# Kernel tuning notes

Measured on AMD Instinct MI355X. Metric: run time of the kernel, lower is better.

The kernel has to match this reference:

```python
import jax, jax.numpy as jnp
import numpy as np

N_NODES = 200000
N_EDGES = 800000
N_GRAPHS = 4096
IN_FEAT = 64
CONV_SIZES = [128, 128, 256, 256]
MAX_DEGREE = 5  # buckets 0..5 (degree clamped)
N_CLASSES = 2


def setup_inputs() -> dict:
    key = jax.random.key(0)
    ks = jax.random.split(key, 32)
    inp = {}
    inp["x"] = jax.random.normal(ks[0], (N_NODES, IN_FEAT), dtype=jnp.float32)
    inp["edge_index"] = jax.random.randint(ks[1], (2, N_EDGES), 0, N_NODES, dtype=jnp.int32)
    inp["batch"] = jnp.sort(jax.random.randint(ks[2], (N_NODES,), 0, N_GRAPHS, dtype=jnp.int32))
    # per-layer MFConv params: Wl (neighbor-sum branch, with bias), Wr (root branch, no bias),
    # one linear per degree bucket -> leading dim MAX_DEGREE+1
    c_in = IN_FEAT
    k = 3
    for li, c_out in enumerate(CONV_SIZES):
        s = 1.0 / np.sqrt(c_in)
        inp[f"Wl{li}"] = jax.random.normal(ks[k], (MAX_DEGREE + 1, c_in, c_out), dtype=jnp.float32) * s; k += 1
        inp[f"bl{li}"] = jax.random.normal(ks[k], (MAX_DEGREE + 1, c_out), dtype=jnp.float32) * 0.01; k += 1
        inp[f"Wr{li}"] = jax.random.normal(ks[k], (MAX_DEGREE + 1, c_in, c_out), dtype=jnp.float32) * s; k += 1
        c_in = c_out
    in_final = sum(CONV_SIZES) + CONV_SIZES[-1]  # concat of all layer outputs + pooled last layer
    inp["Wf"] = jax.random.normal(ks[k], (in_final, N_CLASSES), dtype=jnp.float32) * (1.0 / np.sqrt(in_final)); k += 1
    inp["bf"] = jax.random.normal(ks[k], (N_CLASSES,), dtype=jnp.float32) * 0.01
    return inp


def _mfconv(x, src, dst, deg, Wl, bl, Wr):
    # neighbor sum aggregation (source_to_target flow): msg_i = sum_{j->i} x_j
    msg = jax.ops.segment_sum(x[src], dst, num_segments=x.shape[0])  # [N, c_in]
    out = jnp.zeros((x.shape[0], Wl.shape[2]), dtype=x.dtype)
    for d in range(Wl.shape[0]):  # small fixed loop over degree buckets
        r = msg @ Wl[d] + bl[d] + x @ Wr[d]
        out = jnp.where((deg == d)[:, None], r, out)
    return out


def reference(x, edge_index, batch,
              Wl0, bl0, Wr0, Wl1, bl1, Wr1, Wl2, bl2, Wr2, Wl3, bl3, Wr3,
              Wf, bf):
    src, dst = edge_index[0], edge_index[1]
    n = x.shape[0]
    deg = jnp.clip(jnp.zeros((n,), jnp.int32).at[dst].add(1), 0, MAX_DEGREE)
    hs = []
    h = x
    for Wl, bl, Wr in ((Wl0, bl0, Wr0), (Wl1, bl1, Wr1), (Wl2, bl2, Wr2), (Wl3, bl3, Wr3)):
        h = _mfconv(h, src, dst, deg, Wl, bl, Wr)
        hs.append(h)
    # global_add_pool then repeat_interleave back to nodes == gather pooled by batch id
    h_pool = jax.ops.segment_sum(h, batch, num_segments=N_GRAPHS)  # [G, c_last]
    h_pool_ = h_pool[batch]  # [N, c_last]
    h_cat = jnp.concatenate(hs + [h_pool_], axis=1)  # [N, sum(sizes)+c_last]
    logits = h_cat @ Wf + bf
    return jax.nn.softmax(logits, axis=1)
```

## Files before the change

### kernel.cpp

```cpp
#include <hip/hip_runtime.h>
#include <cstdint>
#include <cstddef>

namespace {

constexpr int NN   = 200000;
constexpr int NE   = 800000;
constexpr int NG   = 4096;
constexpr int MAXD = 5;

constexpr int BM = 64;
constexpr int NBC = (NN + 255) / 256;
constexpr int NBLK  = (NN + BM - 1) / BM + 6;
constexpr int PERMN = NBLK * BM;

typedef _Float16 half8 __attribute__((ext_vector_type(8)));
typedef _Float16 half4 __attribute__((ext_vector_type(4)));
typedef _Float16 half2 __attribute__((ext_vector_type(2)));
typedef float    f32x4 __attribute__((ext_vector_type(4)));

constexpr size_t P_L0 = (size_t)6 * 128 * 128;
constexpr size_t P_L1 = (size_t)6 * 256 * 128;
constexpr size_t P_L2 = (size_t)6 * 256 * 256;
constexpr size_t P_L3 = (size_t)6 * 512 * 256;
constexpr size_t O_P0 = 0;
constexpr size_t O_P1 = O_P0 + P_L0;
constexpr size_t O_P2 = O_P1 + P_L1;
constexpr size_t O_P3 = O_P2 + P_L2;
constexpr size_t WTOT = O_P3 + P_L3;


__global__ void k_memset32(int* __restrict__ p, int v, int n) {
    int i = blockIdx.x * 256 + threadIdx.x;
    if (i < n) p[i] = v;
}

__global__ void k_report(float* __restrict__ outp, float v, int n) {
    int i = blockIdx.x * 256 + threadIdx.x;
    if (i < n) outp[i] = v;
}

template <int CIN, int COUT>
__global__ void k_wpack(const float* __restrict__ Wl, const float* __restrict__ Wr,
                        _Float16* __restrict__ hi, _Float16* __restrict__ lo) {
    constexpr int NT = CIN / 16;
    constexpr int NB = COUT / 16;
    const int total = 6 * NT * NB * 64;
    int idx = blockIdx.x * 256 + threadIdx.x;
    if (idx >= total) return;
    const int lane = idx & 63;
    int rest = idx >> 6;
    const int nb = rest % NB; rest /= NB;
    const int ti = rest % NT;
    const int d  = rest / NT;
    const int k0 = ti * 32 + ((lane >> 4) * 8);
    const int n  = nb * 16 + (lane & 15);
    half8 hv, lv;
#pragma unroll
    for (int j = 0; j < 8; j++) {
        const int kk = k0 + j;
        const float v = (kk < CIN)
                            ? Wl[((size_t)d * CIN + kk) * COUT + n]
                            : Wr[((size_t)d * CIN + (kk - CIN)) * COUT + n];
        const _Float16 h = (_Float16)v;
        hv[j] = h;
        lv[j] = (_Float16)(v - (float)h);
    }
    *(half8*)(hi + (size_t)idx * 8) = hv;
    *(half8*)(lo + (size_t)idx * 8) = lv;
}


__global__ void k_count_deg(const int* __restrict__ dst, int* __restrict__ deg) {
    int e = blockIdx.x * 256 + threadIdx.x;
    if (e < NE) atomicAdd(&deg[dst[e]], 1);
}

__global__ void k_scan_part(const int* __restrict__ deg, int* __restrict__ part) {
    __shared__ int s[256];
    int t = threadIdx.x, i = blockIdx.x * 256 + t;
    s[t] = (i < NN) ? deg[i] : 0;
    __syncthreads();
    for (int st = 128; st > 0; st >>= 1) {
        if (t < st) s[t] += s[t + st];
        __syncthreads();
    }
    if (t == 0) part[blockIdx.x] = s[0];
}

__global__ void k_scan_single(int* __restrict__ part, int nb) {
    __shared__ int s[1024];
    int t = threadIdx.x;
    int v0 = (t < nb) ? part[t] : 0;
    s[t] = v0;
    __syncthreads();
    for (int off = 1; off < 1024; off <<= 1) {
        int v = (t >= off) ? s[t - off] : 0;
        __syncthreads();
        s[t] += v;
        __syncthreads();
    }
    if (t < nb) part[t] = s[t] - v0;
}

__global__ void k_scan_final(const int* __restrict__ deg, const int* __restrict__ part,
                             int* __restrict__ row_ptr, int* __restrict__ cursor) {
    __shared__ int s[256];
    int t = threadIdx.x, i = blockIdx.x * 256 + t;
    int v0 = (i < NN) ? deg[i] : 0;
    s[t] = v0;
    __syncthreads();
    for (int off = 1; off < 256; off <<= 1) {
        int v = (t >= off) ? s[t - off] : 0;
        __syncthreads();
        s[t] += v;
        __syncthreads();
    }
    if (i < NN) {
        int excl = s[t] - v0 + part[blockIdx.x];
        row_ptr[i] = excl;
        cursor[i]  = excl;
        if (i == NN - 1) row_ptr[NN] = excl + v0;
    }
}

__global__ void k_fill_csr(const int* __restrict__ src, const int* __restrict__ dst,
                           int* __restrict__ cursor, int* __restrict__ col) {
    int e = blockIdx.x * 256 + threadIdx.x;
    if (e < NE) {
        int d = dst[e];
        int slot = atomicAdd(&cursor[d], 1);
        col[slot] = src[e];
    }
}


__global__ void k_bucket_blockcount(const int* __restrict__ deg, int* __restrict__ blkcnt) {
    __shared__ int h[6];
    int t = threadIdx.x;
    if (t < 6) h[t] = 0;
    __syncthreads();
    int i = blockIdx.x * 256 + t;
    if (i < NN) atomicAdd(&h[min(deg[i], MAXD)], 1);
    __syncthreads();
    if (t < 6) blkcnt[t * NBC + blockIdx.x] = h[t];
}

__global__ void k_bucket_scanall(int* __restrict__ blkcnt, int* __restrict__ bpad) {
    __shared__ int tot[6];
    int t = threadIdx.x;
    if (t < 6) {
        int run = 0;
        for (int j = 0; j < NBC; j++) {
            int v = blkcnt[t * NBC + j];
            blkcnt[t * NBC + j] = run;
            run += v;
        }
        tot[t] = run;
    }
    __syncthreads();
    if (t == 0) {
        int off = 0;
        for (int b = 0; b < 6; b++) {
            bpad[b] = off;
            off += ((tot[b] + BM - 1) / BM) * BM;
        }
        bpad[6] = off;
    }
}

__global__ void k_scatter2(const int* __restrict__ deg, const int* __restrict__ blkcnt,
                           const int* __restrict__ bpad, int* __restrict__ perm) {
    __shared__ int base[6];
    int t = threadIdx.x;
    if (t < 6) base[t] = bpad[t] + blkcnt[t * NBC + blockIdx.x];
    __syncthreads();
    int i = blockIdx.x * 256 + t;
    if (i < NN) {
        int b = min(deg[i], MAXD);
        int pos = atomicAdd(&base[b], 1);
        perm[pos] = i;
    }
}


__global__ void k_aggregate128(const float* __restrict__ hin, const int* __restrict__ row_ptr,
                               const int* __restrict__ col, float* __restrict__ msg) {
    int node = blockIdx.x * 4 + (threadIdx.x >> 6);
    int lane = threadIdx.x & 63;
    int s = row_ptr[node], e = row_ptr[node + 1];
    float2 acc = make_float2(0.f, 0.f);
    int p = s;
    for (; p + 4 <= e; p += 4) {
        const int c0 = col[p], c1 = col[p + 1], c2 = col[p + 2], c3 = col[p + 3];
        const float2 v0 = *(const float2*)(hin + (size_t)c0 * 128 + lane * 2);
        const float2 v1 = *(const float2*)(hin + (size_t)c1 * 128 + lane * 2);
        const float2 v2 = *(const float2*)(hin + (size_t)c2 * 128 + lane * 2);
        const float2 v3 = *(const float2*)(hin + (size_t)c3 * 128 + lane * 2);
        acc.x += (v0.x + v1.x) + (v2.x + v3.x);
        acc.y += (v0.y + v1.y) + (v2.y + v3.y);
    }
    for (; p < e; p++) {
        const float2 v = *(const float2*)(hin + (size_t)col[p] * 128 + lane * 2);
        acc.x += v.x; acc.y += v.y;
    }
    *(float2*)(msg + (size_t)node * 128 + lane * 2) = acc;
}

template <int C0, int C1, int COUT, int MINW, bool POOL_FUSE>
__launch_bounds__(512, MINW)
__global__ void k_transform(const float* __restrict__ hin0, const float* __restrict__ hin1,
                            const int* __restrict__ row_ptr, const int* __restrict__ col,
                            const _Float16* __restrict__ wph, const _Float16* __restrict__ wpl,
                            const float* __restrict__ bias, const float* __restrict__ Wf,
                            const int* __restrict__ perm, const int* __restrict__ deg,
                            const int* __restrict__ batch,
                            float* __restrict__ out0, float* __restrict__ pool,
                            float* __restrict__ logits, int wf_off) {
    constexpr int CIN = C0 + C1;
    constexpr int NW  = CIN / 32;
    constexpr int NT  = 2 * NW;
    constexpr int NB  = COUT / 16;
    constexpr int NTN = NB / 8;
    constexpr int CPL = CIN / 64;
    constexpr int PB_R = POOL_FUSE ? 64 : 1;
    constexpr int PB_C = 258;

    struct FragBuf {
        _Float16 Ah[NW][4][64][8];
        _Float16 Al[NW][4][64][8];
    };
    union SMemU {
        FragBuf f;
        float pbuf[PB_R][PB_C];
    };
    __shared__ SMemU sm;
    __shared__ int rowid[BM];
    __shared__ int gb[BM];
    __shared__ float lsx[8][BM], lsy[8][BM];

    const int t  = threadIdx.x;
    const int m0 = blockIdx.x * BM;

    if (t < BM) rowid[t] = perm[m0 + t];
    __syncthreads();
    if (rowid[0] < 0) return;

    const int d = min(deg[rowid[0]], MAXD);

    const int am = t & 63, wv = t >> 6;

    if constexpr (POOL_FUSE) {
        if (t < BM) gb[t] = (rowid[t] >= 0) ? batch[rowid[t]] : -1;
    }

    const int kk = CPL * am;
    const bool lo_half = (C1 == 0) || (kk < C0);
    const float* gsrc = lo_half ? hin0 : hin1;
    const int    gst  = lo_half ? C0 : C1;
    const int    goff = lo_half ? kk : (kk - C0);
    const int ti0 = kk >> 5;
    const int o0  = (kk >> 3) & 3;
    const int j00 = kk & 7;

    {
#pragma unroll
        for (int i = 0; i < 8; i++) {
            const int r = wv * 8 + i;
            const int node = rowid[r];
            float a0 = 0.f, a1 = 0.f, a2 = 0.f, a3 = 0.f;
            if (node >= 0) {
                const int es = row_ptr[node], ee = row_ptr[node + 1];
                int p = es;
                for (; p + 4 <= ee; p += 4) {
                    const int c0 = col[p], c1 = col[p + 1];
                    const int c2 = col[p + 2], c3 = col[p + 3];
                    const float* r0 = gsrc + (size_t)c0 * gst + goff;
                    const float* r1 = gsrc + (size_t)c1 * gst + goff;
                    const float* r2 = gsrc + (size_t)c2 * gst + goff;
                    const float* r3 = gsrc + (size_t)c3 * gst + goff;
                    if constexpr (CPL == 4) {
                        f32x4 v0 = *(const f32x4*)r0, v1 = *(const f32x4*)r1;
                        f32x4 v2 = *(const f32x4*)r2, v3 = *(const f32x4*)r3;
                        v0 += v1; v2 += v3; v0 += v2;
                        a0 += v0[0]; a1 += v0[1]; a2 += v0[2]; a3 += v0[3];
                    } else if constexpr (CPL == 2) {
                        float2 v0 = *(const float2*)r0, v1 = *(const float2*)r1;
                        float2 v2 = *(const float2*)r2, v3 = *(const float2*)r3;
                        a0 += (v0.x + v1.x) + (v2.x + v3.x);
                        a1 += (v0.y + v1.y) + (v2.y + v3.y);
                    } else {
                        a0 += (*r0 + *r1) + (*r2 + *r3);
                    }
                }
                for (; p < ee; p++) {
                    const float* rr = gsrc + (size_t)col[p] * gst + goff;
                    if constexpr (CPL == 4) {
                        f32x4 v = *(const f32x4*)rr;
                        a0 += v[0]; a1 += v[1]; a2 += v[2]; a3 += v[3];
                    } else if constexpr (CPL == 2) {
                        float2 v = *(const float2*)rr;
                        a0 += v.x; a1 += v.y;
                    } else {
                        a0 += *rr;
                    }
                }
            }
            const int mt = r >> 4, rl = r & 15;
            if constexpr (CPL == 4) {
                half4 hv, lv;
                hv[0] = (_Float16)a0; lv[0] = (_Float16)(a0 - (float)hv[0]);
                hv[1] = (_Float16)a1; lv[1] = (_Float16)(a1 - (float)hv[1]);
                hv[2] = (_Float16)a2; lv[2] = (_Float16)(a2 - (float)hv[2]);
                hv[3] = (_Float16)a3; lv[3] = (_Float16)(a3 - (float)hv[3]);
                *(half4*)&sm.f.Ah[ti0][mt][rl + 16 * o0][j00] = hv;
                *(half4*)&sm.f.Al[ti0][mt][rl + 16 * o0][j00] = lv;
            } else if constexpr (CPL == 2) {
                half2 hv, lv;
                hv[0] = (_Float16)a0; lv[0] = (_Float16)(a0 - (float)hv[0]);
                hv[1] = (_Float16)a1; lv[1] = (_Float16)(a1 - (float)hv[1]);
                *(half2*)&sm.f.Ah[ti0][mt][rl + 16 * o0][j00] = hv;
                *(half2*)&sm.f.Al[ti0][mt][rl + 16 * o0][j00] = lv;
            } else {
                const _Float16 h = (_Float16)a0;
                sm.f.Ah[ti0][mt][rl + 16 * o0][j00] = h;
                sm.f.Al[ti0][mt][rl + 16 * o0][j00] = (_Float16)(a0 - (float)h);
            }
        }
    }
    __syncthreads();

    const int lx = t & 15, qd = (t >> 4) & 3;
    const int nb0 = wv * NTN;

    f32x4 acc[4][NTN];
#pragma unroll
    for (int mt = 0; mt < 4; mt++)
#pragma unroll
        for (int nt = 0; nt < NTN; nt++) acc[mt][nt] = (f32x4)0.f;

    for (int ti = 0; ti < NW; ti++) {
        half8 bh[NTN], bl[NTN];
        const size_t tbase = (((size_t)d * NT + ti) * NB) * 512;
#pragma unroll
        for (int nt = 0; nt < NTN; nt++) {
            const size_t off = tbase + (size_t)(nb0 + nt) * 512 + (size_t)am * 8;
            bh[nt] = *(const half8*)(wph + off);
            bl[nt] = *(const half8*)(wpl + off);
        }
        half8 ah[4], alo[4];
#pragma unroll
        for (int mt = 0; mt < 4; mt++) {
            ah[mt]  = *(const half8*)&sm.f.Ah[ti][mt][am][0];
            alo[mt] = *(const half8*)&sm.f.Al[ti][mt][am][0];
        }
#pragma unroll
        for (int nt = 0; nt < NTN; nt++)
#pragma unroll
            for (int mt = 0; mt < 4; mt++) {
                acc[mt][nt] = __builtin_amdgcn_mfma_f32_16x16x32_f16(ah[mt],  bh[nt], acc[mt][nt], 0, 0, 0);
                acc[mt][nt] = __builtin_amdgcn_mfma_f32_16x16x32_f16(alo[mt], bh[nt], acc[mt][nt], 0, 0, 0);
                acc[mt][nt] = __builtin_amdgcn_mfma_f32_16x16x32_f16(ah[mt],  bl[nt], acc[mt][nt], 0, 0, 0);
            }
    }
    __syncthreads();

    {
#pragma unroll
        for (int i = 0; i < 8; i++) {
            const int r = wv * 8 + i;
            const int node = rowid[r];
            const int mt = r >> 4, rl = r & 15;
            if constexpr (CPL == 4) {
                f32x4 v = (f32x4)0.f;
                if (node >= 0) v = *(const f32x4*)(gsrc + (size_t)node * gst + goff);
                half4 hv, lv;
#pragma unroll
                for (int c = 0; c < 4; c++) {
                    const _Float16 h = (_Float16)v[c];
                    hv[c] = h; lv[c] = (_Float16)(v[c] - (float)h);
                }
                *(half4*)&sm.f.Ah[ti0][mt][rl + 16 * o0][j00] = hv;
                *(half4*)&sm.f.Al[ti0][mt][rl + 16 * o0][j00] = lv;
            } else if constexpr (CPL == 2) {
                float2 v = make_float2(0.f, 0.f);
                if (node >= 0) v = *(const float2*)(gsrc + (size_t)node * gst + goff);
                half2 hv, lv;
                hv[0] = (_Float16)v.x; lv[0] = (_Float16)(v.x - (float)hv[0]);
                hv[1] = (_Float16)v.y; lv[1] = (_Float16)(v.y - (float)hv[1]);
                *(half2*)&sm.f.Ah[ti0][mt][rl + 16 * o0][j00] = hv;
                *(half2*)&sm.f.Al[ti0][mt][rl + 16 * o0][j00] = lv;
            } else {
                float v = 0.f;
                if (node >= 0) v = gsrc[(size_t)node * gst + goff];
                const _Float16 h = (_Float16)v;
                sm.f.Ah[ti0][mt][rl + 16 * o0][j00] = h;
                sm.f.Al[ti0][mt][rl + 16 * o0][j00] = (_Float16)(v - (float)h);
            }
        }
    }
    __syncthreads();

    for (int ti = 0; ti < NW; ti++) {
        half8 bh[NTN], bl[NTN];
        const size_t tbase = (((size_t)d * NT + NW + ti) * NB) * 512;
#pragma unroll
        for (int nt = 0; nt < NTN; nt++) {
            const size_t off = tbase + (size_t)(nb0 + nt) * 512 + (size_t)am * 8;
            bh[nt] = *(const half8*)(wph + off);
            bl[nt] = *(const half8*)(wpl + off);
        }
        half8 ah[4], alo[4];
#pragma unroll
        for (int mt = 0; mt < 4; mt++) {
            ah[mt]  = *(const half8*)&sm.f.Ah[ti][mt][am][0];
            alo[mt] = *(const half8*)&sm.f.Al[ti][mt][am][0];
        }
#pragma unroll
        for (int nt = 0; nt < NTN; nt++)
#pragma unroll
            for (int mt = 0; mt < 4; mt++) {
                acc[mt][nt] = __builtin_amdgcn_mfma_f32_16x16x32_f16(ah[mt],  bh[nt], acc[mt][nt], 0, 0, 0);
                acc[mt][nt] = __builtin_amdgcn_mfma_f32_16x16x32_f16(alo[mt], bh[nt], acc[mt][nt], 0, 0, 0);
                acc[mt][nt] = __builtin_amdgcn_mfma_f32_16x16x32_f16(ah[mt],  bl[nt], acc[mt][nt], 0, 0, 0);
            }
    }

    float blv[NTN], w0[NTN], w1[NTN];
    int cols[NTN];
#pragma unroll
    for (int nt = 0; nt < NTN; nt++) {
        cols[nt] = wv * (16 * NTN) + nt * 16 + lx;
        blv[nt] = bias[d * COUT + cols[nt]];
        w0[nt]  = Wf[(size_t)(wf_off + cols[nt]) * 2 + 0];
        w1[nt]  = Wf[(size_t)(wf_off + cols[nt]) * 2 + 1];
    }

    __syncthreads();

#pragma unroll
    for (int mt = 0; mt < 4; mt++)
#pragma unroll
    for (int r = 0; r < 4; r++) {
        const int ri = mt * 16 + qd * 4 + r;
        const int node = rowid[ri];
        float p0 = 0.f, p1 = 0.f;
        float h[NTN];
#pragma unroll
        for (int nt = 0; nt < NTN; nt++) h[nt] = 0.f;
        if (node >= 0) {
#pragma unroll
            for (int nt = 0; nt < NTN; nt++) {
                h[nt] = acc[mt][nt][r] + blv[nt];
                p0 = fmaf(h[nt], w0[nt], p0);
                p1 = fmaf(h[nt], w1[nt], p1);
            }
            if constexpr (!POOL_FUSE) {
                float* orow = out0 + (size_t)node * COUT;
#pragma unroll
                for (int nt = 0; nt < NTN; nt++) orow[cols[nt]] = h[nt];
            }
        }
        if constexpr (POOL_FUSE) {
#pragma unroll
            for (int nt = 0; nt < NTN; nt++) sm.pbuf[ri][cols[nt]] = h[nt];
        }
#pragma unroll
        for (int s = 1; s < 16; s <<= 1) {
            p0 += __shfl_xor(p0, s, 64);
            p1 += __shfl_xor(p1, s, 64);
        }
        if (lx == 0) {
            lsx[wv][ri] = p0;
            lsy[wv][ri] = p1;
        }
    }
    __syncthreads();

    if (t < BM) {
        const int node = rowid[t];
        if (node >= 0) {
            float sx = 0.f, sy = 0.f;
#pragma unroll
            for (int w = 0; w < 8; w++) { sx += lsx[w][t]; sy += lsy[w][t]; }
            logits[(size_t)node * 2 + 0] += sx;
            logits[(size_t)node * 2 + 1] += sy;
        }
    }

    if constexpr (POOL_FUSE) {
        const int c  = t & 255;
        const int rh = t >> 8;
        float run = 0.f;
        int rg = -1;
        const int r0 = rh * 32, r1 = r0 + 32;
        for (int r = r0; r < r1; r++) {
            const int g = gb[r];
            if (g != rg) {
                if (rg >= 0) atomicAdd(&pool[(size_t)rg * 256 + c], run);
                run = 0.f; rg = g;
            }
            if (g >= 0) run += sm.pbuf[r][c];
        }
        if (rg >= 0) atomicAdd(&pool[(size_t)rg * 256 + c], run);
    }
}


__launch_bounds__(512, 4)
__global__ void k_gemm2b(float* __restrict__ buf0, float* __restrict__ buf1,
                         const _Float16* __restrict__ wph, const _Float16* __restrict__ wpl,
                         const float* __restrict__ bias, const float* __restrict__ Wf,
                         const int* __restrict__ perm, const int* __restrict__ deg,
                         float* __restrict__ logits) {
    constexpr int COUT = 256, NT = 8, NB = 16, NTN = 2;
    __shared__ _Float16 Ah[NT][4][64][8];
    __shared__ _Float16 Al[NT][4][64][8];
    __shared__ int rowid[BM];
    __shared__ float lsx[8][BM], lsy[8][BM];

    const int t  = threadIdx.x;
    const int m0 = blockIdx.x * BM;

    if (t < BM) rowid[t] = perm[m0 + t];
    __syncthreads();
    if (rowid[0] < 0) return;

    const int d = min(deg[rowid[0]], MAXD);

    const int am = t & 63, wv = t >> 6;

    {
        const int kk = 4 * am;
        const float* gsrc = (am < 32) ? buf0 : buf1;
        const int    goff = (am < 32) ? kk : (kk - 128);
        const int ti = am >> 3;
        const int o  = (am >> 1) & 3;
        const int j0 = 4 * (am & 1);
#pragma unroll
        for (int i = 0; i < 8; i++) {
            const int r = wv * 8 + i;
            const int node = rowid[r];
            f32x4 v = (f32x4)0.f;
            if (node >= 0) v = *(const f32x4*)(gsrc + (size_t)node * 128 + goff);
            const int mt = r >> 4, rl = r & 15;
            half4 hv, lv;
#pragma unroll
            for (int c = 0; c < 4; c++) {
                const _Float16 h = (_Float16)v[c];
                hv[c] = h; lv[c] = (_Float16)(v[c] - (float)h);
            }
            *(half4*)&Ah[ti][mt][rl + 16 * o][j0] = hv;
            *(half4*)&Al[ti][mt][rl + 16 * o][j0] = lv;
        }
    }
    __syncthreads();

    const int lx = t & 15, qd = (t >> 4) & 3;
    const int nb0 = wv * NTN;

    f32x4 acc[4][NTN];
#pragma unroll
    for (int mt = 0; mt < 4; mt++)
#pragma unroll
        for (int nt = 0; nt < NTN; nt++) acc[mt][nt] = (f32x4)0.f;

    for (int ti = 0; ti < NT; ti++) {
        half8 bh[NTN], bl[NTN];
        const size_t tbase = (((size_t)d * NT + ti) * NB) * 512;
#pragma unroll
        for (int nt = 0; nt < NTN; nt++) {
            const size_t off = tbase + (size_t)(nb0 + nt) * 512 + (size_t)am * 8;
            bh[nt] = *(const half8*)(wph + off);
            bl[nt] = *(const half8*)(wpl + off);
        }
        half8 ah[4], alo[4];
#pragma unroll
        for (int mt = 0; mt < 4; mt++) {
            ah[mt]  = *(const half8*)&Ah[ti][mt][am][0];
            alo[mt] = *(const half8*)&Al[ti][mt][am][0];
        }
#pragma unroll
        for (int nt = 0; nt < NTN; nt++)
#pragma unroll
            for (int mt = 0; mt < 4; mt++) {
                acc[mt][nt] = __builtin_amdgcn_mfma_f32_16x16x32_f16(ah[mt],  bh[nt], acc[mt][nt], 0, 0, 0);
                acc[mt][nt] = __builtin_amdgcn_mfma_f32_16x16x32_f16(alo[mt], bh[nt], acc[mt][nt], 0, 0, 0);
                acc[mt][nt] = __builtin_amdgcn_mfma_f32_16x16x32_f16(ah[mt],  bl[nt], acc[mt][nt], 0, 0, 0);
            }
    }

    float blv[NTN], w0[NTN], w1[NTN];
    int cols[NTN];
#pragma unroll
    for (int nt = 0; nt < NTN; nt++) {
        cols[nt] = wv * 32 + nt * 16 + lx;
        blv[nt] = bias[d * COUT + cols[nt]];
        w0[nt]  = Wf[(size_t)(256 + cols[nt]) * 2 + 0];
        w1[nt]  = Wf[(size_t)(256 + cols[nt]) * 2 + 1];
    }
#pragma unroll
    for (int mt = 0; mt < 4; mt++)
#pragma unroll
    for (int r = 0; r < 4; r++) {
        const int ri = mt * 16 + qd * 4 + r;
        const int node = rowid[ri];
        float p0 = 0.f, p1 = 0.f;
        if (node >= 0) {
#pragma unroll
            for (int nt = 0; nt < NTN; nt++) {
                const float h = acc[mt][nt][r] + blv[nt];
                p0 = fmaf(h, w0[nt], p0);
                p1 = fmaf(h, w1[nt], p1);
                if (cols[nt] < 128) buf0[(size_t)node * 128 + cols[nt]] = h;
                else                buf1[(size_t)node * 128 + cols[nt] - 128] = h;
            }
        }
#pragma unroll
        for (int s = 1; s < 16; s <<= 1) {
            p0 += __shfl_xor(p0, s, 64);
            p1 += __shfl_xor(p1, s, 64);
        }
        if (lx == 0) {
            lsx[wv][ri] = p0;
            lsy[wv][ri] = p1;
        }
    }
    __syncthreads();
    if (t < BM) {
        const int node = rowid[t];
        if (node >= 0) {
            float sx = 0.f, sy = 0.f;
#pragma unroll
            for (int w = 0; w < 8; w++) { sx += lsx[w][t]; sy += lsy[w][t]; }
            logits[(size_t)node * 2 + 0] += sx;
            logits[(size_t)node * 2 + 1] += sy;
        }
    }
}


__global__ void k_pool_logits(const float* __restrict__ pool, const float* __restrict__ Wf,
                              const float* __restrict__ bf, float* __restrict__ pl) {
    int g = blockIdx.x * 4 + (threadIdx.x >> 6);
    int lane = threadIdx.x & 63;
    const float* pr = pool + (size_t)g * 256;
    float p0 = 0.f, p1 = 0.f;
#pragma unroll
    for (int j = 0; j < 4; j++) {
        int k = lane + 64 * j;
        float v = pr[k];
        p0 = fmaf(v, Wf[(size_t)(768 + k) * 2 + 0], p0);
        p1 = fmaf(v, Wf[(size_t)(768 + k) * 2 + 1], p1);
    }
#pragma unroll
    for (int s = 1; s < 64; s <<= 1) {
        p0 += __shfl_xor(p0, s, 64);
        p1 += __shfl_xor(p1, s, 64);
    }
    if (lane == 0) {
        pl[(size_t)g * 2 + 0] = p0 + bf[0];
        pl[(size_t)g * 2 + 1] = p1 + bf[1];
    }
}

__global__ void k_final(const float* __restrict__ logits, const float* __restrict__ pl,
                        const int* __restrict__ batch, float* __restrict__ outp) {
    int i = blockIdx.x * 256 + threadIdx.x;
    if (i < NN) {
        int g = batch[i];
        float l0 = logits[(size_t)i * 2 + 0] + pl[(size_t)g * 2 + 0];
        float l1 = logits[(size_t)i * 2 + 1] + pl[(size_t)g * 2 + 1];
        float m = fmaxf(l0, l1);
        float e0 = expf(l0 - m), e1 = expf(l1 - m);
        float inv = 1.f / (e0 + e1);
        outp[(size_t)i * 2 + 0] = e0 * inv;
        outp[(size_t)i * 2 + 1] = e1 * inv;
    }
}

}

extern "C" void kernel_launch(void* const* d_in, const int* in_sizes, int n_in,
                              void* d_out, int out_size, void* d_ws, size_t ws_size,
                              hipStream_t stream) {
    const float* x     = (const float*)d_in[0];
    const int*   ei    = (const int*)d_in[1];
    const int*   batch = (const int*)d_in[2];
    const float* Wl0 = (const float*)d_in[3];  const float* bl0 = (const float*)d_in[4];
    const float* Wr0 = (const float*)d_in[5];
    const float* Wl1 = (const float*)d_in[6];  const float* bl1 = (const float*)d_in[7];
    const float* Wr1 = (const float*)d_in[8];
    const float* Wl2 = (const float*)d_in[9];  const float* bl2 = (const float*)d_in[10];
    const float* Wr2 = (const float*)d_in[11];
    const float* Wl3 = (const float*)d_in[12]; const float* bl3 = (const float*)d_in[13];
    const float* Wr3 = (const float*)d_in[14];
    const float* Wf  = (const float*)d_in[15]; const float* bf  = (const float*)d_in[16];
    const int* src = ei;
    const int* dst = ei + NE;
    float* outp = (float*)d_out;
    (void)in_sizes; (void)n_in;

    char* w = (char*)d_ws;
    auto alloc = [&](size_t bytes) -> void* {
        void* p = (void*)w;
        w += (bytes + 255) & ~(size_t)255;
        return p;
    };
    int*   deg    = (int*)alloc((size_t)NN * 4);
    float* logits = (float*)alloc((size_t)NN * 2 * 4);
    float* pool   = (float*)alloc((size_t)NG * 256 * 4);
    size_t zero_words = (size_t)(w - (char*)deg) / 4;
    int*   bpad    = (int*)alloc(32);
    int*   blkcnt  = (int*)alloc((size_t)6 * NBC * 4);
    int*   perm    = (int*)alloc((size_t)PERMN * 4);
    int*   row_ptr = (int*)alloc((size_t)(NN + 1) * 4);
    int*   cursor  = (int*)alloc((size_t)NN * 4);
    int*   col     = (int*)alloc((size_t)NE * 4);
    int*   part    = (int*)alloc(1024 * 4);
    float* pl      = (float*)alloc((size_t)NG * 2 * 4);
    _Float16* whi  = (_Float16*)alloc(WTOT * 2);
    _Float16* wlo  = (_Float16*)alloc(WTOT * 2);
    float* bufA    = (float*)alloc((size_t)NN * 128 * 4);
    float* bufB    = (float*)alloc((size_t)NN * 128 * 4);

    size_t required = (size_t)(w - (char*)d_ws);
    if (required > ws_size) {
        k_report<<<(out_size + 255) / 256, 256, 0, stream>>>(
            outp, (float)(double)(ws_size >> 20), out_size);
        return;
    }

    dim3 b256(256);
    dim3 b512(512);
    k_memset32<<<(int)((zero_words + 255) / 256), b256, 0, stream>>>((int*)deg, 0, (int)zero_words);
    k_memset32<<<(PERMN + 255) / 256, b256, 0, stream>>>(perm, -1, PERMN);

    k_wpack<64, 128><<<(int)(P_L0 / 8 + 255) / 256, b256, 0, stream>>>(Wl0, Wr0, whi + O_P0, wlo + O_P0);
    k_wpack<128, 128><<<(int)(P_L1 / 8 + 255) / 256, b256, 0, stream>>>(Wl1, Wr1, whi + O_P1, wlo + O_P1);
    k_wpack<128, 256><<<(int)(P_L2 / 8 + 255) / 256, b256, 0, stream>>>(Wl2, Wr2, whi + O_P2, wlo + O_P2);
    k_wpack<256, 256><<<(int)(P_L3 / 8 + 255) / 256, b256, 0, stream>>>(Wl3, Wr3, whi + O_P3, wlo + O_P3);

    k_count_deg<<<NE / 256, b256, 0, stream>>>(dst, deg);
    k_scan_part<<<NBC, b256, 0, stream>>>(deg, part);
    k_scan_single<<<1, 1024, 0, stream>>>(part, NBC);
    k_scan_final<<<NBC, b256, 0, stream>>>(deg, part, row_ptr, cursor);
    k_fill_csr<<<NE / 256, b256, 0, stream>>>(src, dst, cursor, col);
    k_bucket_blockcount<<<NBC, b256, 0, stream>>>(deg, blkcnt);
    k_bucket_scanall<<<1, 64, 0, stream>>>(blkcnt, bpad);
    k_scatter2<<<NBC, b256, 0, stream>>>(deg, blkcnt, bpad, perm);

    k_transform<64, 0, 128, 4, false><<<dim3(NBLK), b512, 0, stream>>>(
        x, nullptr, row_ptr, col, whi + O_P0, wlo + O_P0,
        bl0, Wf, perm, deg, nullptr, bufA, nullptr, logits, 0);
    k_transform<128, 0, 128, 4, false><<<dim3(NBLK), b512, 0, stream>>>(
        bufA, nullptr, row_ptr, col, whi + O_P1, wlo + O_P1,
        bl1, Wf, perm, deg, nullptr, bufB, nullptr, logits, 128);
    k_aggregate128<<<NN / 4, b256, 0, stream>>>(bufB, row_ptr, col, bufA);
    k_gemm2b<<<dim3(NBLK), b512, 0, stream>>>(
        bufA, bufB, whi + O_P2, wlo + O_P2, bl2, Wf, perm, deg, logits);
    k_transform<128, 128, 256, 4, true><<<dim3(NBLK), b512, 0, stream>>>(
        bufA, bufB, row_ptr, col, whi + O_P3, wlo + O_P3,
        bl3, Wf, perm, deg, batch, nullptr, pool, logits, 512);

    k_pool_logits<<<NG / 4, b256, 0, stream>>>(pool, Wf, bf, pl);
    k_final<<<NBC, b256, 0, stream>>>(logits, pl, batch, outp);
}
```

Before: 1.209 ms.

## Split K-dimension staging into 128-wide phases to shrink LDS and raise occupancy

The transform and gemm2b kernels now stage the A operand through shared memory in 128-column phases instead of the full input width. This cuts the LDS footprint, and the pooling buffer is halved to 32 rows processed in two passes. Launch bounds rise from 4 to 8 waves per SIMD, aiming for more resident blocks to hide gather latency. In exchange there are extra barriers per phase, the neighbor gathers are repeated once per phase, and fewer registers are available per thread, which could cause spills.

```diff
diff --git a/kernel.cpp b/kernel.cpp
--- a/kernel.cpp
+++ b/kernel.cpp
@@ -222,13 +222,16 @@
     constexpr int NT  = 2 * NW;
     constexpr int NB  = COUT / 16;
     constexpr int NTN = NB / 8;
-    constexpr int CPL = CIN / 64;
-    constexpr int PB_R = POOL_FUSE ? 64 : 1;
+    constexpr int PHW = (CIN >= 128) ? (CIN / 128) : 1;
+    constexpr int KW  = CIN / PHW;
+    constexpr int CPLp = KW / 64;
+    constexpr int NWP = KW / 32;
+    constexpr int PB_R = POOL_FUSE ? 32 : 1;
     constexpr int PB_C = 258;
 
     struct FragBuf {
-        _Float16 Ah[NW][4][64][8];
-        _Float16 Al[NW][4][64][8];
+        _Float16 Ah[NWP][4][64][8];
+        _Float16 Al[NWP][4][64][8];
     };
     union SMemU {
         FragBuf f;
@@ -254,37 +257,40 @@
         if (t < BM) gb[t] = (rowid[t] >= 0) ? batch[rowid[t]] : -1;
     }
 
-    const int kk = CPL * am;
-    const bool lo_half = (C1 == 0) || (kk < C0);
-    const float* gsrc = lo_half ? hin0 : hin1;
-    const int    gst  = lo_half ? C0 : C1;
-    const int    goff = lo_half ? kk : (kk - C0);
-    const int ti0 = kk >> 5;
-    const int o0  = (kk >> 3) & 3;
-    const int j00 = kk & 7;
-
-    {
+    const int kk  = CPLp * am;
+    const int tiL = kk >> 5;
+    const int oL  = (kk >> 3) & 3;
+    const int jL  = kk & 7;
+
+    const int lx = t & 15, qd = (t >> 4) & 3;
+    const int nb0 = wv * NTN;
+
+    f32x4 acc[4][NTN];
+#pragma unroll
+    for (int mt = 0; mt < 4; mt++)
+#pragma unroll
+        for (int nt = 0; nt < NTN; nt++) acc[mt][nt] = (f32x4)0.f;
+
+#pragma unroll
+    for (int p = 0; p < PHW; p++) {
+        const float* src = (C1 != 0 && p == 1) ? hin1 : hin0;
+        const int    str = (C1 != 0 && p == 1) ? C1 : C0;
 #pragma unroll
         for (int i = 0; i < 8; i++) {
             const int r = wv * 8 + i;
             const int node = rowid[r];
-            float a0 = 0.f, a1 = 0.f, a2 = 0.f, a3 = 0.f;
+            float a0 = 0.f, a1 = 0.f;
             if (node >= 0) {
                 const int es = row_ptr[node], ee = row_ptr[node + 1];
-                int p = es;
-                for (; p + 4 <= ee; p += 4) {
-                    const int c0 = col[p], c1 = col[p + 1];
-                    const int c2 = col[p + 2], c3 = col[p + 3];
-                    const float* r0 = gsrc + (size_t)c0 * gst + goff;
-                    const float* r1 = gsrc + (size_t)c1 * gst + goff;
-                    const float* r2 = gsrc + (size_t)c2 * gst + goff;
-                    const float* r3 = gsrc + (size_t)c3 * gst + goff;
-                    if constexpr (CPL == 4) {
-                        f32x4 v0 = *(const f32x4*)r0, v1 = *(const f32x4*)r1;
-                        f32x4 v2 = *(const f32x4*)r2, v3 = *(const f32x4*)r3;
-                        v0 += v1; v2 += v3; v0 += v2;
-                        a0 += v0[0]; a1 += v0[1]; a2 += v0[2]; a3 += v0[3];
-                    } else if constexpr (CPL == 2) {
+                int pp = es;
+                for (; pp + 4 <= ee; pp += 4) {
+                    const int c0 = col[pp], c1 = col[pp + 1];
+                    const int c2 = col[pp + 2], c3 = col[pp + 3];
+                    const float* r0 = src + (size_t)c0 * str + kk;
+                    const float* r1 = src + (size_t)c1 * str + kk;
+                    const float* r2 = src + (size_t)c2 * str + kk;
+                    const float* r3 = src + (size_t)c3 * str + kk;
+                    if constexpr (CPLp == 2) {
                         float2 v0 = *(const float2*)r0, v1 = *(const float2*)r1;
                         float2 v2 = *(const float2*)r2, v3 = *(const float2*)r3;
                         a0 += (v0.x + v1.x) + (v2.x + v3.x);
@@ -293,12 +299,9 @@
                         a0 += (*r0 + *r1) + (*r2 + *r3);
                     }
                 }
-                for (; p < ee; p++) {
-                    const float* rr = gsrc + (size_t)col[p] * gst + goff;
-                    if constexpr (CPL == 4) {
-                        f32x4 v = *(const f32x4*)rr;
-                        a0 += v[0]; a1 += v[1]; a2 += v[2]; a3 += v[3];
-                    } else if constexpr (CPL == 2) {
+                for (; pp < ee; pp++) {
+                    const float* rr = src + (size_t)col[pp] * str + kk;
+                    if constexpr (CPLp == 2) {
                         float2 v = *(const float2*)rr;
                         a0 += v.x; a1 += v.y;
                     } else {
@@ -307,123 +310,97 @@
                 }
             }
             const int mt = r >> 4, rl = r & 15;
-            if constexpr (CPL == 4) {
-                half4 hv, lv;
-                hv[0] = (_Float16)a0; lv[0] = (_Float16)(a0 - (float)hv[0]);
-                hv[1] = (_Float16)a1; lv[1] = (_Float16)(a1 - (float)hv[1]);
-                hv[2] = (_Float16)a2; lv[2] = (_Float16)(a2 - (float)hv[2]);
-                hv[3] = (_Float16)a3; lv[3] = (_Float16)(a3 - (float)hv[3]);
-                *(half4*)&sm.f.Ah[ti0][mt][rl + 16 * o0][j00] = hv;
-                *(half4*)&sm.f.Al[ti0][mt][rl + 16 * o0][j00] = lv;
-            } else if constexpr (CPL == 2) {
+            if constexpr (CPLp == 2) {
                 half2 hv, lv;
                 hv[0] = (_Float16)a0; lv[0] = (_Float16)(a0 - (float)hv[0]);
                 hv[1] = (_Float16)a1; lv[1] = (_Float16)(a1 - (float)hv[1]);
-                *(half2*)&sm.f.Ah[ti0][mt][rl + 16 * o0][j00] = hv;
-                *(half2*)&sm.f.Al[ti0][mt][rl + 16 * o0][j00] = lv;
+                *(half2*)&sm.f.Ah[tiL][mt][rl + 16 * oL][jL] = hv;
+                *(half2*)&sm.f.Al[tiL][mt][rl + 16 * oL][jL] = lv;
             } else {
                 const _Float16 h = (_Float16)a0;
-                sm.f.Ah[ti0][mt][rl + 16 * o0][j00] = h;
-                sm.f.Al[ti0][mt][rl + 16 * o0][j00] = (_Float16)(a0 - (float)h);
-            }
-        }
-    }
-    __syncthreads();
-
-    const int lx = t & 15, qd = (t >> 4) & 3;
-    const int nb0 = wv * NTN;
-
-    f32x4 acc[4][NTN];
-#pragma unroll
-    for (int mt = 0; mt < 4; mt++)
-#pragma unroll
-        for (int nt = 0; nt < NTN; nt++) acc[mt][nt] = (f32x4)0.f;
-
-    for (int ti = 0; ti < NW; ti++) {
-        half8 bh[NTN], bl[NTN];
-        const size_t tbase = (((size_t)d * NT + ti) * NB) * 512;
-#pragma unroll
-        for (int nt = 0; nt < NTN; nt++) {
-            const size_t off = tbase + (size_t)(nb0 + nt) * 512 + (size_t)am * 8;
-            bh[nt] = *(const half8*)(wph + off);
-            bl[nt] = *(const half8*)(wpl + off);
-        }
-        half8 ah[4], alo[4];
-#pragma unroll
-        for (int mt = 0; mt < 4; mt++) {
-            ah[mt]  = *(const half8*)&sm.f.Ah[ti][mt][am][0];
-            alo[mt] = *(const half8*)&sm.f.Al[ti][mt][am][0];
-        }
-#pragma unroll
-        for (int nt = 0; nt < NTN; nt++)
+                sm.f.Ah[tiL][mt][rl + 16 * oL][jL] = h;
+                sm.f.Al[tiL][mt][rl + 16 * oL][jL] = (_Float16)(a0 - (float)h);
+            }
+        }
+        __syncthreads();
+        for (int ti = 0; ti < NWP; ti++) {
+            half8 bh[NTN], bl[NTN];
+            const size_t tbase = (((size_t)d * NT + (p * NWP + ti)) * NB) * 512;
+#pragma unroll
+            for (int nt = 0; nt < NTN; nt++) {
+                const size_t off = tbase + (size_t)(nb0 + nt) * 512 + (size_t)am * 8;
+                bh[nt] = *(const half8*)(wph + off);
+                bl[nt] = *(const half8*)(wpl + off);
+            }
+            half8 ah[4], alo[4];
 #pragma unroll
             for (int mt = 0; mt < 4; mt++) {
-                acc[mt][nt] = __builtin_amdgcn_mfma_f32_16x16x32_f16(ah[mt],  bh[nt], acc[mt][nt], 0, 0, 0);
-                acc[mt][nt] = __builtin_amdgcn_mfma_f32_16x16x32_f16(alo[mt], bh[nt], acc[mt][nt], 0, 0, 0);
-                acc[mt][nt] = __builtin_amdgcn_mfma_f32_16x16x32_f16(ah[mt],  bl[nt], acc[mt][nt], 0, 0, 0);
-            }
-    }
-    __syncthreads();
-
-    {
+                ah[mt]  = *(const half8*)&sm.f.Ah[ti][mt][am][0];
+                alo[mt] = *(const half8*)&sm.f.Al[ti][mt][am][0];
+            }
+#pragma unroll
+            for (int nt = 0; nt < NTN; nt++)
+#pragma unroll
+                for (int mt = 0; mt < 4; mt++) {
+                    acc[mt][nt] = __builtin_amdgcn_mfma_f32_16x16x32_f16(ah[mt],  bh[nt], acc[mt][nt], 0, 0, 0);
+                    acc[mt][nt] = __builtin_amdgcn_mfma_f32_16x16x32_f16(alo[mt], bh[nt], acc[mt][nt], 0, 0, 0);
+                    acc[mt][nt] = __builtin_amdgcn_mfma_f32_16x16x32_f16(ah[mt],  bl[nt], acc[mt][nt], 0, 0, 0);
+                }
+        }
+        __syncthreads();
+    }
+
+#pragma unroll
+    for (int p = 0; p < PHW; p++) {
+        const float* src = (C1 != 0 && p == 1) ? hin1 : hin0;
+        const int    str = (C1 != 0 && p == 1) ? C1 : C0;
 #pragma unroll
         for (int i = 0; i < 8; i++) {
             const int r = wv * 8 + i;
             const int node = rowid[r];
             const int mt = r >> 4, rl = r & 15;
-            if constexpr (CPL == 4) {
-                f32x4 v = (f32x4)0.f;
-                if (node >= 0) v = *(const f32x4*)(gsrc + (size_t)node * gst + goff);
-                half4 hv, lv;
-#pragma unroll
-                for (int c = 0; c < 4; c++) {
-                    const _Float16 h = (_Float16)v[c];
-                    hv[c] = h; lv[c] = (_Float16)(v[c] - (float)h);
-                }
-                *(half4*)&sm.f.Ah[ti0][mt][rl + 16 * o0][j00] = hv;
-                *(half4*)&sm.f.Al[ti0][mt][rl + 16 * o0][j00] = lv;
-            } else if constexpr (CPL == 2) {
+            if constexpr (CPLp == 2) {
                 float2 v = make_float2(0.f, 0.f);
-                if (node >= 0) v = *(const float2*)(gsrc + (size_t)node * gst + goff);
+                if (node >= 0) v = *(const float2*)(src + (size_t)node * str + kk);
                 half2 hv, lv;
                 hv[0] = (_Float16)v.x; lv[0] = (_Float16)(v.x - (float)hv[0]);
                 hv[1] = (_Float16)v.y; lv[1] = (_Float16)(v.y - (float)hv[1]);
-                *(half2*)&sm.f.Ah[ti0][mt][rl + 16 * o0][j00] = hv;
-                *(half2*)&sm.f.Al[ti0][mt][rl + 16 * o0][j00] = lv;
+                *(half2*)&sm.f.Ah[tiL][mt][rl + 16 * oL][jL] = hv;
+                *(half2*)&sm.f.Al[tiL][mt][rl + 16 * oL][jL] = lv;
             } else {
                 float v = 0.f;
-                if (node >= 0) v = gsrc[(size_t)node * gst + goff];
+                if (node >= 0) v = src[(size_t)node * str + kk];
                 const _Float16 h = (_Float16)v;
-                sm.f.Ah[ti0][mt][rl + 16 * o0][j00] = h;
-                sm.f.Al[ti0][mt][rl + 16 * o0][j00] = (_Float16)(v - (float)h);
-            }
-        }
-    }
-    __syncthreads();
-
-    for (int ti = 0; ti < NW; ti++) {
-        half8 bh[NTN], bl[NTN];
-        const size_t tbase = (((size_t)d * NT + NW + ti) * NB) * 512;
-#pragma unroll
-        for (int nt = 0; nt < NTN; nt++) {
-            const size_t off = tbase + (size_t)(nb0 + nt) * 512 + (size_t)am * 8;
-            bh[nt] = *(const half8*)(wph + off);
-            bl[nt] = *(const half8*)(wpl + off);
-        }
-        half8 ah[4], alo[4];
-#pragma unroll
-        for (int mt = 0; mt < 4; mt++) {
-            ah[mt]  = *(const half8*)&sm.f.Ah[ti][mt][am][0];
-            alo[mt] = *(const half8*)&sm.f.Al[ti][mt][am][0];
-        }
-#pragma unroll
-        for (int nt = 0; nt < NTN; nt++)
+                sm.f.Ah[tiL][mt][rl + 16 * oL][jL] = h;
+                sm.f.Al[tiL][mt][rl + 16 * oL][jL] = (_Float16)(v - (float)h);
+            }
+        }
+        __syncthreads();
+        for (int ti = 0; ti < NWP; ti++) {
+            half8 bh[NTN], bl[NTN];
+            const size_t tbase = (((size_t)d * NT + (NW + p * NWP + ti)) * NB) * 512;
+#pragma unroll
+            for (int nt = 0; nt < NTN; nt++) {
+                const size_t off = tbase + (size_t)(nb0 + nt) * 512 + (size_t)am * 8;
+                bh[nt] = *(const half8*)(wph + off);
+                bl[nt] = *(const half8*)(wpl + off);
+            }
+            half8 ah[4], alo[4];
 #pragma unroll
             for (int mt = 0; mt < 4; mt++) {
-                acc[mt][nt] = __builtin_amdgcn_mfma_f32_16x16x32_f16(ah[mt],  bh[nt], acc[mt][nt], 0, 0, 0);
-                acc[mt][nt] = __builtin_amdgcn_mfma_f32_16x16x32_f16(alo[mt], bh[nt], acc[mt][nt], 0, 0, 0);
-                acc[mt][nt] = __builtin_amdgcn_mfma_f32_16x16x32_f16(ah[mt],  bl[nt], acc[mt][nt], 0, 0, 0);
-            }
+                ah[mt]  = *(const half8*)&sm.f.Ah[ti][mt][am][0];
+                alo[mt] = *(const half8*)&sm.f.Al[ti][mt][am][0];
+            }
+#pragma unroll
+            for (int nt = 0; nt < NTN; nt++)
+#pragma unroll
+                for (int mt = 0; mt < 4; mt++) {
+                    acc[mt][nt] = __builtin_amdgcn_mfma_f32_16x16x32_f16(ah[mt],  bh[nt], acc[mt][nt], 0, 0, 0);
+                    acc[mt][nt] = __builtin_amdgcn_mfma_f32_16x16x32_f16(alo[mt], bh[nt], acc[mt][nt], 0, 0, 0);
+                    acc[mt][nt] = __builtin_amdgcn_mfma_f32_16x16x32_f16(ah[mt],  bl[nt], acc[mt][nt], 0, 0, 0);
+                }
+        }
+        __syncthreads();
     }
 
     float blv[NTN], w0[NTN], w1[NTN];
@@ -436,8 +413,6 @@
         w1[nt]  = Wf[(size_t)(wf_off + cols[nt]) * 2 + 1];
     }
 
-    __syncthreads();
-
 #pragma unroll
     for (int mt = 0; mt < 4; mt++)
 #pragma unroll
@@ -445,25 +420,19 @@
         const int ri = mt * 16 + qd * 4 + r;
         const int node = rowid[ri];
         float p0 = 0.f, p1 = 0.f;
-        float h[NTN];
-#pragma unroll
-        for (int nt = 0; nt < NTN; nt++) h[nt] = 0.f;
         if (node >= 0) {
 #pragma unroll
             for (int nt = 0; nt < NTN; nt++) {
-                h[nt] = acc[mt][nt][r] + blv[nt];
-                p0 = fmaf(h[nt], w0[nt], p0);
-                p1 = fmaf(h[nt], w1[nt], p1);
+                const float h = acc[mt][nt][r] + blv[nt];
+                p0 = fmaf(h, w0[nt], p0);
+                p1 = fmaf(h, w1[nt], p1);
             }
             if constexpr (!POOL_FUSE) {
                 float* orow = out0 + (size_t)node * COUT;
 #pragma unroll
-                for (int nt = 0; nt < NTN; nt++) orow[cols[nt]] = h[nt];
-            }
-        }
-        if constexpr (POOL_FUSE) {
-#pragma unroll
-            for (int nt = 0; nt < NTN; nt++) sm.pbuf[ri][cols[nt]] = h[nt];
+                for (int nt = 0; nt < NTN; nt++)
+                    orow[cols[nt]] = acc[mt][nt][r] + blv[nt];
+            }
         }
 #pragma unroll
         for (int s = 1; s < 16; s <<= 1) {
@@ -489,33 +458,51 @@
     }
 
     if constexpr (POOL_FUSE) {
-        const int c  = t & 255;
-        const int rh = t >> 8;
-        float run = 0.f;
-        int rg = -1;
-        const int r0 = rh * 32, r1 = r0 + 32;
-        for (int r = r0; r < r1; r++) {
-            const int g = gb[r];
-            if (g != rg) {
+#pragma unroll
+        for (int half = 0; half < 2; half++) {
+#pragma unroll
+            for (int mt = 2 * half; mt < 2 * half + 2; mt++)
+#pragma unroll
+            for (int r = 0; r < 4; r++) {
+                const int ri = mt * 16 + qd * 4 + r;
+                const int node = rowid[ri];
+#pragma unroll
+                for (int nt = 0; nt < NTN; nt++)
+                    sm.pbuf[ri - 32 * half][cols[nt]] =
+                        (node >= 0) ? (acc[mt][nt][r] + blv[nt]) : 0.f;
+            }
+            __syncthreads();
+            {
+                const int c  = t & 255;
+                const int rh = t >> 8;
+                float run = 0.f;
+                int rg = -1;
+                const int r0 = rh * 16, r1 = r0 + 16;
+                for (int rr = r0; rr < r1; rr++) {
+                    const int g = gb[32 * half + rr];
+                    if (g != rg) {
+                        if (rg >= 0) atomicAdd(&pool[(size_t)rg * 256 + c], run);
+                        run = 0.f; rg = g;
+                    }
+                    if (g >= 0) run += sm.pbuf[rr][c];
+                }
                 if (rg >= 0) atomicAdd(&pool[(size_t)rg * 256 + c], run);
-                run = 0.f; rg = g;
-            }
-            if (g >= 0) run += sm.pbuf[r][c];
-        }
-        if (rg >= 0) atomicAdd(&pool[(size_t)rg * 256 + c], run);
-    }
-}
-
-
-__launch_bounds__(512, 4)
+            }
+            __syncthreads();
+        }
+    }
+}
+
+
+__launch_bounds__(512, 8)
 __global__ void k_gemm2b(float* __restrict__ buf0, float* __restrict__ buf1,
                          const _Float16* __restrict__ wph, const _Float16* __restrict__ wpl,
                          const float* __restrict__ bias, const float* __restrict__ Wf,
                          const int* __restrict__ perm, const int* __restrict__ deg,
                          float* __restrict__ logits) {
-    constexpr int COUT = 256, NT = 8, NB = 16, NTN = 2;
-    __shared__ _Float16 Ah[NT][4][64][8];
-    __shared__ _Float16 Al[NT][4][64][8];
+    constexpr int COUT = 256, NT = 8, NB = 16, NTN = 2, NWP = 4;
+    __shared__ _Float16 Ah[NWP][4][64][8];
+    __shared__ _Float16 Al[NWP][4][64][8];
     __shared__ int rowid[BM];
     __shared__ float lsx[8][BM], lsy[8][BM];
 
@@ -528,35 +515,10 @@
 
     const int d = min(deg[rowid[0]], MAXD);
 
-    const int am = t & 63, wv = t >> 6;
-
-    {
-        const int kk = 4 * am;
-        const float* gsrc = (am < 32) ? buf0 : buf1;
-        const int    goff = (am < 32) ? kk : (kk - 128);
-        const int ti = am >> 3;
-        const int o  = (am >> 1) & 3;
-        const int j0 = 4 * (am & 1);
-#pragma unroll
-        for (int i = 0; i < 8; i++) {
-            const int r = wv * 8 + i;
-            const int node = rowid[r];
-            f32x4 v = (f32x4)0.f;
-            if (node >= 0) v = *(const f32x4*)(gsrc + (size_t)node * 128 + goff);
-            const int mt = r >> 4, rl = r & 15;
-            half4 hv, lv;
-#pragma unroll
-            for (int c = 0; c < 4; c++) {
-                const _Float16 h = (_Float16)v[c];
-                hv[c] = h; lv[c] = (_Float16)(v[c] - (float)h);
-            }
-            *(half4*)&Ah[ti][mt][rl + 16 * o][j0] = hv;
-            *(half4*)&Al[ti][mt][rl + 16 * o][j0] = lv;
-        }
-    }
-    __syncthreads();
-
-    const int lx = t & 15, qd = (t >> 4) & 3;
+    const int am = t & 63, aq = t >> 6;
+    const int anode = rowid[am];
+    const int mt_w = am >> 4, rl = am & 15;
+    const int lx = t & 15, qd = (t >> 4) & 3, wv = t >> 6;
     const int nb0 = wv * NTN;
 
     f32x4 acc[4][NTN];
@@ -565,29 +527,60 @@
 #pragma unroll
         for (int nt = 0; nt < NTN; nt++) acc[mt][nt] = (f32x4)0.f;
 
-    for (int ti = 0; ti < NT; ti++) {
-        half8 bh[NTN], bl[NTN];
-        const size_t tbase = (((size_t)d * NT + ti) * NB) * 512;
-#pragma unroll
-        for (int nt = 0; nt < NTN; nt++) {
-            const size_t off = tbase + (size_t)(nb0 + nt) * 512 + (size_t)am * 8;
-            bh[nt] = *(const half8*)(wph + off);
-            bl[nt] = *(const half8*)(wpl + off);
-        }
-        half8 ah[4], alo[4];
-#pragma unroll
-        for (int mt = 0; mt < 4; mt++) {
-            ah[mt]  = *(const half8*)&Ah[ti][mt][am][0];
-            alo[mt] = *(const half8*)&Al[ti][mt][am][0];
-        }
-#pragma unroll
-        for (int nt = 0; nt < NTN; nt++)
+#pragma unroll
+    for (int p = 0; p < 2; p++) {
+        {
+            const int k0 = 16 * aq;
+            f32x4 v[4];
+#pragma unroll
+            for (int u = 0; u < 4; u++) v[u] = (f32x4)0.f;
+            if (anode >= 0) {
+                const float* r = (p == 0 ? buf0 : buf1) + (size_t)anode * 128 + k0;
+#pragma unroll
+                for (int u = 0; u < 4; u++) v[u] = *(const f32x4*)(r + 4 * u);
+            }
+#pragma unroll
+            for (int u = 0; u < 4; u++) {
+                const int kL = k0 + 4 * u;
+                const int ti = kL >> 5;
+                const int o  = (kL >> 3) & 3;
+                const int j0 = kL & 7;
+                half4 hv, lv;
+#pragma unroll
+                for (int i = 0; i < 4; i++) {
+                    const _Float16 h = (_Float16)v[u][i];
+                    hv[i] = h; lv[i] = (_Float16)(v[u][i] - (float)h);
+                }
+                *(half4*)&Ah[ti][mt_w][rl + 16 * o][j0] = hv;
+                *(half4*)&Al[ti][mt_w][rl + 16 * o][j0] = lv;
+            }
+        }
+        __syncthreads();
+        for (int ti = 0; ti < NWP; ti++) {
+            half8 bh[NTN], bl[NTN];
+            const size_t tbase = (((size_t)d * NT + (p * NWP + ti)) * NB) * 512;
+#pragma unroll
+            for (int nt = 0; nt < NTN; nt++) {
+                const size_t off = tbase + (size_t)(nb0 + nt) * 512 + (size_t)am * 8;
+                bh[nt] = *(const half8*)(wph + off);
+                bl[nt] = *(const half8*)(wpl + off);
+            }
+            half8 ah[4], alo[4];
 #pragma unroll
             for (int mt = 0; mt < 4; mt++) {
-                acc[mt][nt] = __builtin_amdgcn_mfma_f32_16x16x32_f16(ah[mt],  bh[nt], acc[mt][nt], 0, 0, 0);
-                acc[mt][nt] = __builtin_amdgcn_mfma_f32_16x16x32_f16(alo[mt], bh[nt], acc[mt][nt], 0, 0, 0);
-                acc[mt][nt] = __builtin_amdgcn_mfma_f32_16x16x32_f16(ah[mt],  bl[nt], acc[mt][nt], 0, 0, 0);
-            }
+                ah[mt]  = *(const half8*)&Ah[ti][mt][am][0];
+                alo[mt] = *(const half8*)&Al[ti][mt][am][0];
+            }
+#pragma unroll
+            for (int nt = 0; nt < NTN; nt++)
+#pragma unroll
+                for (int mt = 0; mt < 4; mt++) {
+                    acc[mt][nt] = __builtin_amdgcn_mfma_f32_16x16x32_f16(ah[mt],  bh[nt], acc[mt][nt], 0, 0, 0);
+                    acc[mt][nt] = __builtin_amdgcn_mfma_f32_16x16x32_f16(alo[mt], bh[nt], acc[mt][nt], 0, 0, 0);
+                    acc[mt][nt] = __builtin_amdgcn_mfma_f32_16x16x32_f16(ah[mt],  bl[nt], acc[mt][nt], 0, 0, 0);
+                }
+        }
+        __syncthreads();
     }
 
     float blv[NTN], w0[NTN], w1[NTN];
@@ -750,16 +743,16 @@
     k_bucket_scanall<<<1, 64, 0, stream>>>(blkcnt, bpad);
     k_scatter2<<<NBC, b256, 0, stream>>>(deg, blkcnt, bpad, perm);
 
-    k_transform<64, 0, 128, 4, false><<<dim3(NBLK), b512, 0, stream>>>(
+    k_transform<64, 0, 128, 8, false><<<dim3(NBLK), b512, 0, stream>>>(
         x, nullptr, row_ptr, col, whi + O_P0, wlo + O_P0,
         bl0, Wf, perm, deg, nullptr, bufA, nullptr, logits, 0);
-    k_transform<128, 0, 128, 4, false><<<dim3(NBLK), b512, 0, stream>>>(
+    k_transform<128, 0, 128, 8, false><<<dim3(NBLK), b512, 0, stream>>>(
         bufA, nullptr, row_ptr, col, whi + O_P1, wlo + O_P1,
         bl1, Wf, perm, deg, nullptr, bufB, nullptr, logits, 128);
     k_aggregate128<<<NN / 4, b256, 0, stream>>>(bufB, row_ptr, col, bufA);
     k_gemm2b<<<dim3(NBLK), b512, 0, stream>>>(
         bufA, bufB, whi + O_P2, wlo + O_P2, bl2, Wf, perm, deg, logits);
-    k_transform<128, 128, 256, 4, true><<<dim3(NBLK), b512, 0, stream>>>(
+    k_transform<128, 128, 256, 8, true><<<dim3(NBLK), b512, 0, stream>>>(
         bufA, bufB, row_ptr, col, whi + O_P3, wlo + O_P3,
         bl3, Wf, perm, deg, batch, nullptr, pool, logits, 512);
 
```

After: 2.637 ms. 118% more time.
